# Optimization experiments

Measured on AMD Instinct MI355X. Metric: run time of the kernel, lower is better.

Reference implementation:

```python
import jax, jax.numpy as jnp
import numpy as np

EMB = 1024
HEADS = 16
DH = EMB // HEADS


def setup_inputs() -> dict:
    key = jax.random.key(0)
    ks = jax.random.split(key, 9)
    B, S = 4, 2048
    scale = 1.0 / np.sqrt(EMB)
    x = jax.random.normal(ks[0], (B, S, EMB), dtype=jnp.float32)
    Wq = jax.random.normal(ks[1], (EMB, EMB), dtype=jnp.float32) * scale
    Wk = jax.random.normal(ks[2], (EMB, EMB), dtype=jnp.float32) * scale
    Wv = jax.random.normal(ks[3], (EMB, EMB), dtype=jnp.float32) * scale
    Wo = jax.random.normal(ks[4], (EMB, EMB), dtype=jnp.float32) * scale
    bq = jnp.zeros((EMB,), jnp.float32)
    bk = jnp.zeros((EMB,), jnp.float32)
    bv = jnp.zeros((EMB,), jnp.float32)
    bo = jnp.zeros((EMB,), jnp.float32)
    return {"x": x, "Wq": Wq, "bq": bq, "Wk": Wk, "bk": bk,
            "Wv": Wv, "bv": bv, "Wo": Wo, "bo": bo}


def _split_heads(t):
    B, S, _ = t.shape
    return t.reshape(B, S, HEADS, DH).transpose(0, 2, 1, 3)  # [B,H,S,Dh]


def reference(x, Wq, bq, Wk, bk, Wv, bv, Wo, bo):
    q = _split_heads(x @ Wq + bq)
    k = _split_heads(x @ Wk + bk)
    v = _split_heads(x @ Wv + bv)
    # scaled dot-product attention, full [B,H,S,S] score matrix as in source
    logits = jnp.einsum("bhqd,bhkd->bhqk", q, k) / jnp.sqrt(jnp.float32(DH))
    attn = jax.nn.softmax(logits, axis=-1)
    ctx = jnp.einsum("bhqk,bhkd->bhqd", attn, v)
    B, _, S, _ = ctx.shape
    concat = ctx.transpose(0, 2, 1, 3).reshape(B, S, EMB)
    return concat @ Wo + bo
```

## Files before the change

kernel.cpp:

```cpp
#include <hip/hip_runtime.h>
#include <hip/hip_bf16.h>
#include <stdint.h>

typedef __bf16 bf16;
typedef __bf16 bf16x4 __attribute__((ext_vector_type(4)));
typedef __bf16 bf16x8 __attribute__((ext_vector_type(8)));
typedef float f32x4 __attribute__((ext_vector_type(4)));

__device__ __forceinline__ void async_ld16(const void* g, void* l) {
  __builtin_amdgcn_global_load_lds(
      (__attribute__((address_space(1))) void*)(void*)(g),
      (__attribute__((address_space(3))) void*)(l), 16, 0, 0);
}

__device__ __forceinline__ bf16 fast_bf16(float f) {
  uint32_t u = (__float_as_uint(f) + 0x8000u) >> 16;
  union { uint16_t s; bf16 b; } cv;
  cv.s = (uint16_t)u;
  return cv.b;
}

__device__ __forceinline__ uint32_t pack_bf16(float lo, float hi) {
  return __builtin_amdgcn_perm(__float_as_uint(hi) + 0x8000u,
                               __float_as_uint(lo) + 0x8000u, 0x07060302u);
}

__global__ __launch_bounds__(256) void cast_f32_bf16(const float* __restrict__ in,
                                                     bf16* __restrict__ out, int n) {
  int i = (blockIdx.x * 256 + threadIdx.x) * 4;
  if (i < n) {
    float4 f = *(const float4*)(in + i);
    uint2 o;
    o.x = pack_bf16(f.x, f.y);
    o.y = pack_bf16(f.z, f.w);
    *(uint2*)(out + i) = o;
  }
}

__global__ __launch_bounds__(256) void transpose_weights(const float* __restrict__ Wq,
                                                         const float* __restrict__ Wk,
                                                         const float* __restrict__ Wv,
                                                         const float* __restrict__ Wo,
                                                         bf16* __restrict__ Wt,
                                                         bf16* __restrict__ Wot) {
  __shared__ bf16 tile[64][66];
  int z = blockIdx.z;
  const float* src = z == 0 ? Wq : (z == 1 ? Wk : (z == 2 ? Wv : Wo));
  bf16* dst = z == 0 ? Wt : (z == 1 ? Wt + 1048576 : (z == 2 ? Wt + 2097152 : Wot));
  int r0 = blockIdx.x * 64, c0 = blockIdx.y * 64;
  int t = threadIdx.x;
#pragma unroll
  for (int i = 0; i < 16; ++i) {
    int idx = t + i * 256;
    int r = idx >> 6, c = idx & 63;
    tile[r][c] = fast_bf16(src[(size_t)(r0 + r) * 1024 + (c0 + c)]);
  }
  __syncthreads();
#pragma unroll
  for (int i = 0; i < 16; ++i) {
    int idx = t + i * 256;
    int c = idx >> 6, r = idx & 63;
    dst[(size_t)(c0 + c) * 1024 + (r0 + r)] = tile[r][c];
  }
}

__device__ __forceinline__ void gemm128_mainloop(const bf16* __restrict__ A,
                                                 const bf16* __restrict__ Bt, int K,
                                                 int rowBase, int colBase,
                                                 bf16* As, bf16* Bs,
                                                 f32x4 (&acc)[4][4]) {
  int t = threadIdx.x, lane = t & 63, w = t >> 6;
  int wM = w >> 1, wN = w & 1, quad = lane >> 4, l15 = lane & 15;
  int r_off = lane >> 3;
  int c_sw = (((lane & 7) ^ r_off) << 3);
  int sw = l15 & 7;
  for (int k0 = 0; k0 < K; k0 += 64) {
    __syncthreads();
#pragma unroll
    for (int i = 0; i < 4; ++i) {
      int e = i * 2048 + w * 512;
      int row = (e >> 6) + r_off;
      async_ld16(A + (size_t)(rowBase + row) * K + (k0 + c_sw), As + e);
      async_ld16(Bt + (size_t)(colBase + row) * K + (k0 + c_sw), Bs + e);
    }
    __syncthreads();
#pragma unroll
    for (int ks = 0; ks < 2; ++ks) {
      int co = (((ks * 4 + quad) ^ sw) << 3);
      bf16x8 af[4], bfr[4];
#pragma unroll
      for (int mi = 0; mi < 4; ++mi)
        af[mi] = *(const bf16x8*)(As + (wM * 64 + mi * 16 + l15) * 64 + co);
#pragma unroll
      for (int ni = 0; ni < 4; ++ni)
        bfr[ni] = *(const bf16x8*)(Bs + (wN * 64 + ni * 16 + l15) * 64 + co);
#pragma unroll
      for (int mi = 0; mi < 4; ++mi)
#pragma unroll
        for (int ni = 0; ni < 4; ++ni)
          acc[mi][ni] = __builtin_amdgcn_mfma_f32_16x16x32_bf16(af[mi], bfr[ni], acc[mi][ni], 0, 0, 0);
    }
  }
}

__global__ __launch_bounds__(256) void gemm_qkv(const bf16* __restrict__ X,
                                                const bf16* __restrict__ Wt,
                                                const float* __restrict__ bq,
                                                const float* __restrict__ bk,
                                                const float* __restrict__ bv,
                                                bf16* __restrict__ Qo,
                                                bf16* __restrict__ Ko,
                                                bf16* __restrict__ Vto) {
  __shared__ alignas(16) bf16 smem[2 * 128 * 64];
  bf16* As = smem;
  bf16* Bs = smem + 128 * 64;
  f32x4 acc[4][4];
  f32x4 z = {0.f, 0.f, 0.f, 0.f};
#pragma unroll
  for (int mi = 0; mi < 4; ++mi)
#pragma unroll
    for (int ni = 0; ni < 4; ++ni) acc[mi][ni] = z;
  int rowBase = blockIdx.y * 128, colBase = blockIdx.x * 128;
  gemm128_mainloop(X, Wt, 1024, rowBase, colBase, As, Bs, acc);

  int t = threadIdx.x, lane = t & 63, w = t >> 6;
  int wM = w >> 1, wN = w & 1, quad = lane >> 4, l15 = lane & 15;
  int which = colBase >> 10;
  int baseh = (colBase & 1023) >> 6;
  int b = rowBase >> 11, s0 = rowBase & 2047;

  if (which == 2) {
#pragma unroll
    for (int hp = 0; hp < 2; ++hp) {
      __syncthreads();
      if (wN == hp) {
#pragma unroll
        for (int mi = 0; mi < 4; ++mi)
#pragma unroll
          for (int ni = 0; ni < 4; ++ni) {
            int d = ni * 16 + l15;
            float bb = bv[(colBase & 1023) + hp * 64 + d];
            int sl = wM * 64 + mi * 16 + quad * 4;
            uint2 pv;
            pv.x = pack_bf16(acc[mi][ni][0] + bb, acc[mi][ni][1] + bb);
            pv.y = pack_bf16(acc[mi][ni][2] + bb, acc[mi][ni][3] + bb);
            *(uint2*)(smem + d * 136 + sl) = pv;
          }
      }
      __syncthreads();
      int hg = baseh + hp;
#pragma unroll
      for (int it = 0; it < 4; ++it) {
        int idx = t + it * 256;
        int d = idx >> 4, c = idx & 15;
        bf16x8 vv = *(const bf16x8*)(smem + d * 136 + c * 8);
        *(bf16x8*)(Vto + (((size_t)((b << 4) + hg) << 6) + d) * 2048 + s0 + c * 8) = vv;
      }
    }
  } else {
    const float* bias = which == 0 ? bq : bk;
    bf16* dst = which == 0 ? Qo : Ko;
    float scale = which == 0 ? 0.125f * 1.44269504f : 1.0f;
#pragma unroll
    for (int hp = 0; hp < 2; ++hp) {
      __syncthreads();
      if (wN == hp) {
#pragma unroll
        for (int mi = 0; mi < 4; ++mi)
#pragma unroll
          for (int ni = 0; ni < 4; ++ni) {
            int d = ni * 16 + l15;
            float bb = bias[(colBase & 1023) + hp * 64 + d];
            int m = wM * 64 + mi * 16 + quad * 4;
#pragma unroll
            for (int r = 0; r < 4; ++r)
              smem[(m + r) * 72 + d] = fast_bf16((acc[mi][ni][r] + bb) * scale);
          }
      }
      __syncthreads();
      int hg = baseh + hp;
      bf16* gbase = dst + ((((size_t)((b << 4) + hg)) * 2048 + s0) << 6);
#pragma unroll
      for (int it = 0; it < 4; ++it) {
        int idx = t + it * 256;
        int m = idx >> 3, c = idx & 7;
        bf16x8 vv = *(const bf16x8*)(smem + m * 72 + c * 8);
        *(bf16x8*)(gbase + m * 64 + c * 8) = vv;
      }
    }
  }
}

__global__ __launch_bounds__(256) void gemm_out(const bf16* __restrict__ Cb,
                                                const bf16* __restrict__ Wot,
                                                const float* __restrict__ bo,
                                                float* __restrict__ out) {
  __shared__ alignas(16) bf16 As[128 * 64];
  __shared__ alignas(16) bf16 Bs[128 * 64];
  f32x4 acc[4][4];
  f32x4 z = {0.f, 0.f, 0.f, 0.f};
#pragma unroll
  for (int mi = 0; mi < 4; ++mi)
#pragma unroll
    for (int ni = 0; ni < 4; ++ni) acc[mi][ni] = z;
  int rowBase = blockIdx.y * 128, colBase = blockIdx.x * 128;
  gemm128_mainloop(Cb, Wot, 1024, rowBase, colBase, As, Bs, acc);

  int t = threadIdx.x, lane = t & 63, w = t >> 6;
  int wM = w >> 1, wN = w & 1, quad = lane >> 4, l15 = lane & 15;
#pragma unroll
  for (int mi = 0; mi < 4; ++mi)
#pragma unroll
    for (int ni = 0; ni < 4; ++ni) {
      int n = colBase + wN * 64 + ni * 16 + l15;
      float bb = bo[n];
#pragma unroll
      for (int r = 0; r < 4; ++r) {
        int m = rowBase + wM * 64 + mi * 16 + quad * 4 + r;
        out[(size_t)m * 1024 + n] = acc[mi][ni][r] + bb;
      }
    }
}

__global__ __launch_bounds__(256, 2) void attn(const bf16* __restrict__ Q,
                                               const bf16* __restrict__ Kg,
                                               const bf16* __restrict__ Vt,
                                               bf16* __restrict__ ctx) {
  __shared__ alignas(16) bf16 QPs[256 * 64];
  __shared__ alignas(16) bf16 Ks[2][4096];
  __shared__ alignas(16) bf16 Vs[2][4096];

  int t = threadIdx.x, lane = t & 63, w = t >> 6;
  int quad = lane >> 4, l15 = lane & 15;
  int r_off = lane >> 3;
  int c_sw = (((lane & 7) ^ r_off) << 3);
  int sw = l15 & 7;
  int bh = blockIdx.x;
  int q0 = blockIdx.y * 256;
  const bf16* Qp = Q + ((size_t)bh * 2048 + q0) * 64;
  const bf16* Kp = Kg + (size_t)bh * 2048 * 64;
  const bf16* Vp = Vt + (size_t)bh * 64 * 2048;

#pragma unroll
  for (int i = 0; i < 8; ++i) {
    int e = w * 4096 + i * 512;
    int row = (e >> 6) + r_off;
    async_ld16(Qp + (size_t)row * 64 + c_sw, QPs + e);
  }
#pragma unroll
  for (int i = 0; i < 2; ++i) {
    int e = w * 1024 + i * 512;
    int row = (e >> 6) + r_off;
    async_ld16(Kp + (size_t)row * 64 + c_sw, Ks[0] + e);
    async_ld16(Vp + (size_t)row * 2048 + c_sw, Vs[0] + e);
  }
  __syncthreads();

  bf16x8 qf[2][4];
#pragma unroll
  for (int ks = 0; ks < 2; ++ks)
#pragma unroll
    for (int qi = 0; qi < 4; ++qi)
      qf[ks][qi] = *(const bf16x8*)(QPs + (w * 64 + qi * 16 + l15) * 64 + (((ks * 4 + quad) ^ sw) << 3));
  asm volatile("s_waitcnt lgkmcnt(0)" ::: "memory");

  bf16* Ps = QPs + w * 4096;

  bf16 one1 = (bf16)1.0f;
  bf16x8 ones = {one1, one1, one1, one1, one1, one1, one1, one1};

  f32x4 o[4][4];
  f32x4 ol[4];
  f32x4 z = {0.f, 0.f, 0.f, 0.f};
#pragma unroll
  for (int mi = 0; mi < 4; ++mi) {
    ol[mi] = z;
#pragma unroll
    for (int ni = 0; ni < 4; ++ni) o[mi][ni] = z;
  }

  for (int kt = 0; kt < 32; ++kt) {
    int cur = kt & 1;
    if (kt < 31) {
      int kn = (kt + 1) * 64;
#pragma unroll
      for (int i = 0; i < 2; ++i) {
        int e = w * 1024 + i * 512;
        int row = (e >> 6) + r_off;
        async_ld16(Kp + (size_t)(kn + row) * 64 + c_sw, Ks[cur ^ 1] + e);
        async_ld16(Vp + (size_t)row * 2048 + kn + c_sw, Vs[cur ^ 1] + e);
      }
    }
    const bf16* Kc = Ks[cur];
    const bf16* Vc = Vs[cur];

    f32x4 sA[2][4];
#pragma unroll
    for (int ki = 0; ki < 2; ++ki)
#pragma unroll
      for (int qi = 0; qi < 4; ++qi) sA[ki][qi] = z;
    __builtin_amdgcn_s_setprio(1);
#pragma unroll
    for (int ks = 0; ks < 2; ++ks) {
      int co = (((ks * 4 + quad) ^ sw) << 3);
      bf16x8 kf0 = *(const bf16x8*)(Kc + (l15) * 64 + co);
      bf16x8 kf1 = *(const bf16x8*)(Kc + (16 + l15) * 64 + co);
#pragma unroll
      for (int qi = 0; qi < 4; ++qi) {
        sA[0][qi] = __builtin_amdgcn_mfma_f32_16x16x32_bf16(kf0, qf[ks][qi], sA[0][qi], 0, 0, 0);
        sA[1][qi] = __builtin_amdgcn_mfma_f32_16x16x32_bf16(kf1, qf[ks][qi], sA[1][qi], 0, 0, 0);
      }
    }
    __builtin_amdgcn_s_setprio(0);
#pragma unroll
    for (int qi = 0; qi < 4; ++qi)
#pragma unroll
      for (int ki = 0; ki < 2; ++ki) {
        float p0 = __builtin_amdgcn_exp2f(sA[ki][qi][0]);
        float p1 = __builtin_amdgcn_exp2f(sA[ki][qi][1]);
        float p2 = __builtin_amdgcn_exp2f(sA[ki][qi][2]);
        float p3 = __builtin_amdgcn_exp2f(sA[ki][qi][3]);
        uint2 pb;
        pb.x = pack_bf16(p0, p1);
        pb.y = pack_bf16(p2, p3);
        int cs = (ki * 2 + (quad >> 1)) ^ sw;
        *(uint2*)(Ps + (qi * 16 + l15) * 64 + cs * 8 + (quad & 1) * 4) = pb;
      }

    f32x4 sB[2][4];
#pragma unroll
    for (int ki = 0; ki < 2; ++ki)
#pragma unroll
      for (int qi = 0; qi < 4; ++qi) sB[ki][qi] = z;
    __builtin_amdgcn_s_setprio(1);
#pragma unroll
    for (int ks = 0; ks < 2; ++ks) {
      int co = (((ks * 4 + quad) ^ sw) << 3);
      bf16x8 kf2 = *(const bf16x8*)(Kc + (32 + l15) * 64 + co);
      bf16x8 kf3 = *(const bf16x8*)(Kc + (48 + l15) * 64 + co);
#pragma unroll
      for (int qi = 0; qi < 4; ++qi) {
        sB[0][qi] = __builtin_amdgcn_mfma_f32_16x16x32_bf16(kf2, qf[ks][qi], sB[0][qi], 0, 0, 0);
        sB[1][qi] = __builtin_amdgcn_mfma_f32_16x16x32_bf16(kf3, qf[ks][qi], sB[1][qi], 0, 0, 0);
      }
    }
    __builtin_amdgcn_s_setprio(0);

    asm volatile("s_waitcnt lgkmcnt(0)" ::: "memory");

    {
      int co = ((quad ^ sw) << 3);
      bf16x8 pf[4], vf[4];
#pragma unroll
      for (int mi = 0; mi < 4; ++mi)
        pf[mi] = *(const bf16x8*)(Ps + (mi * 16 + l15) * 64 + co);
#pragma unroll
      for (int ni = 0; ni < 4; ++ni)
        vf[ni] = *(const bf16x8*)(Vc + (ni * 16 + l15) * 64 + co);
      __builtin_amdgcn_s_setprio(1);
#pragma unroll
      for (int mi = 0; mi < 4; ++mi) {
#pragma unroll
        for (int ni = 0; ni < 4; ++ni)
          o[mi][ni] = __builtin_amdgcn_mfma_f32_16x16x32_bf16(pf[mi], vf[ni], o[mi][ni], 0, 0, 0);
        ol[mi] = __builtin_amdgcn_mfma_f32_16x16x32_bf16(pf[mi], ones, ol[mi], 0, 0, 0);
      }
      __builtin_amdgcn_s_setprio(0);
    }

#pragma unroll
    for (int qi = 0; qi < 4; ++qi)
#pragma unroll
      for (int ki = 0; ki < 2; ++ki) {
        float p0 = __builtin_amdgcn_exp2f(sB[ki][qi][0]);
        float p1 = __builtin_amdgcn_exp2f(sB[ki][qi][1]);
        float p2 = __builtin_amdgcn_exp2f(sB[ki][qi][2]);
        float p3 = __builtin_amdgcn_exp2f(sB[ki][qi][3]);
        uint2 pb;
        pb.x = pack_bf16(p0, p1);
        pb.y = pack_bf16(p2, p3);
        int cs = (ki * 2 + 4 + (quad >> 1)) ^ sw;
        *(uint2*)(Ps + (qi * 16 + l15) * 64 + cs * 8 + (quad & 1) * 4) = pb;
      }

    asm volatile("s_waitcnt lgkmcnt(0)" ::: "memory");

    {
      int co = (((4 + quad) ^ sw) << 3);
      bf16x8 pf[4], vf[4];
#pragma unroll
      for (int mi = 0; mi < 4; ++mi)
        pf[mi] = *(const bf16x8*)(Ps + (mi * 16 + l15) * 64 + co);
#pragma unroll
      for (int ni = 0; ni < 4; ++ni)
        vf[ni] = *(const bf16x8*)(Vc + (ni * 16 + l15) * 64 + co);
      __builtin_amdgcn_s_setprio(1);
#pragma unroll
      for (int mi = 0; mi < 4; ++mi) {
#pragma unroll
        for (int ni = 0; ni < 4; ++ni)
          o[mi][ni] = __builtin_amdgcn_mfma_f32_16x16x32_bf16(pf[mi], vf[ni], o[mi][ni], 0, 0, 0);
        ol[mi] = __builtin_amdgcn_mfma_f32_16x16x32_bf16(pf[mi], ones, ol[mi], 0, 0, 0);
      }
      __builtin_amdgcn_s_setprio(0);
    }

    __syncthreads();
  }

  int b = bh >> 4, h = bh & 15;
#pragma unroll
  for (int mi = 0; mi < 4; ++mi) {
    float rl[4];
#pragma unroll
    for (int r = 0; r < 4; ++r) rl[r] = 1.0f / ol[mi][r];
#pragma unroll
    for (int ni = 0; ni < 4; ++ni) {
      int col = h * 64 + ni * 16 + l15;
#pragma unroll
      for (int r = 0; r < 4; ++r) {
        int q = q0 + w * 64 + mi * 16 + quad * 4 + r;
        ctx[(size_t)(b * 2048 + q) * 1024 + col] = fast_bf16(o[mi][ni][r] * rl[r]);
      }
    }
  }
}

extern "C" void kernel_launch(void* const* d_in, const int* in_sizes, int n_in,
                              void* d_out, int out_size, void* d_ws, size_t ws_size,
                              hipStream_t stream) {
  const float* x  = (const float*)d_in[0];
  const float* Wq = (const float*)d_in[1];
  const float* bq = (const float*)d_in[2];
  const float* Wk = (const float*)d_in[3];
  const float* bk = (const float*)d_in[4];
  const float* Wv = (const float*)d_in[5];
  const float* bv = (const float*)d_in[6];
  const float* Wo = (const float*)d_in[7];
  const float* bo = (const float*)d_in[8];
  float* out = (float*)d_out;

  char* ws = (char*)d_ws;
  const size_t MB = 1048576;
  bf16* xb  = (bf16*)(ws);
  bf16* Wt  = (bf16*)(ws + 16 * MB);
  bf16* Wot = (bf16*)(ws + 22 * MB);
  bf16* Qb  = (bf16*)(ws + 24 * MB);
  bf16* Kb  = (bf16*)(ws + 40 * MB);
  bf16* Vtb = (bf16*)(ws + 56 * MB);
  bf16* Cx  = (bf16*)(ws + 72 * MB);

  cast_f32_bf16<<<8192, 256, 0, stream>>>(x, xb, 8388608);
  transpose_weights<<<dim3(16, 16, 4), 256, 0, stream>>>(Wq, Wk, Wv, Wo, Wt, Wot);
  gemm_qkv<<<dim3(24, 64, 1), 256, 0, stream>>>(xb, Wt, bq, bk, bv, Qb, Kb, Vtb);
  attn<<<dim3(64, 8, 1), 256, 0, stream>>>(Qb, Kb, Vtb, Cx);
  gemm_out<<<dim3(8, 64, 1), 256, 0, stream>>>(Cx, Wot, bo, out);
}
```

Measured before the change: 280.6 us.

## Double-buffer QKV GEMM with 256x128 tiles and interleaved async loads

Reworks the QKV projection GEMM to use 256x128 output tiles with 512 threads. It double-buffers the A and B tiles in LDS and issues the next k-step's async global-to-LDS loads between MFMA sub-phases. MFMA bursts are wrapped in sched_barrier and setprio to keep the matrix units busy while loads are in flight. The epilogue is adapted to the larger tile. The aim is to hide global load latency and raise operand reuse per block, at the cost of about 96KB of LDS per block, which limits occupancy.

```diff
diff --git a/kernel.cpp b/kernel.cpp
--- a/kernel.cpp
+++ b/kernel.cpp
@@ -103,31 +103,143 @@
   }
 }
 
-__global__ __launch_bounds__(256) void gemm_qkv(const bf16* __restrict__ X,
-                                                const bf16* __restrict__ Wt,
-                                                const float* __restrict__ bq,
-                                                const float* __restrict__ bk,
-                                                const float* __restrict__ bv,
-                                                bf16* __restrict__ Qo,
-                                                bf16* __restrict__ Ko,
-                                                bf16* __restrict__ Vto) {
-  __shared__ alignas(16) bf16 smem[2 * 128 * 64];
-  bf16* As = smem;
-  bf16* Bs = smem + 128 * 64;
+__global__ __launch_bounds__(512, 2) void gemm_qkv(const bf16* __restrict__ X,
+                                                   const bf16* __restrict__ Wt,
+                                                   const float* __restrict__ bq,
+                                                   const float* __restrict__ bk,
+                                                   const float* __restrict__ bv,
+                                                   bf16* __restrict__ Qo,
+                                                   bf16* __restrict__ Ko,
+                                                   bf16* __restrict__ Vto) {
+  __shared__ alignas(16) bf16 smem[2][24576];
+
+  int t = threadIdx.x, lane = t & 63, w = t >> 6;
+  int wM = w >> 1, wN = w & 1, quad = lane >> 4, l15 = lane & 15;
+  int r_off = lane >> 3;
+  int c_sw = (((lane & 7) ^ r_off) << 3);
+  int sw = l15 & 7;
+  int rowBase = blockIdx.y * 256, colBase = blockIdx.x * 128;
+
   f32x4 acc[4][4];
   f32x4 z = {0.f, 0.f, 0.f, 0.f};
 #pragma unroll
   for (int mi = 0; mi < 4; ++mi)
 #pragma unroll
     for (int ni = 0; ni < 4; ++ni) acc[mi][ni] = z;
-  int rowBase = blockIdx.y * 128, colBase = blockIdx.x * 128;
-  gemm128_mainloop(X, Wt, 1024, rowBase, colBase, As, Bs, acc);
-
-  int t = threadIdx.x, lane = t & 63, w = t >> 6;
-  int wM = w >> 1, wN = w & 1, quad = lane >> 4, l15 = lane & 15;
+
+#pragma unroll
+  for (int i = 0; i < 4; ++i) {
+    int e = (w * 4 + i) * 512;
+    int row = (e >> 6) + r_off;
+    async_ld16(X + (size_t)(rowBase + row) * 1024 + c_sw, smem[0] + e);
+  }
+#pragma unroll
+  for (int i = 0; i < 2; ++i) {
+    int e = (w * 2 + i) * 512;
+    int row = (e >> 6) + r_off;
+    async_ld16(Wt + (size_t)(colBase + row) * 1024 + c_sw, smem[0] + 16384 + e);
+  }
+  __syncthreads();
+
+  for (int kt = 0; kt < 16; ++kt) {
+    int cur = kt & 1;
+    const bf16* As = smem[cur];
+    const bf16* Bs = smem[cur] + 16384;
+    bf16* Asn = smem[cur ^ 1];
+    bf16* Bsn = smem[cur ^ 1] + 16384;
+    int kn = (kt + 1) * 64;
+
+    bf16x8 af[4], bfr[2];
+
+    if (kt < 15) {
+#pragma unroll
+      for (int i = 0; i < 4; ++i) {
+        int e = (w * 4 + i) * 512;
+        int row = (e >> 6) + r_off;
+        async_ld16(X + (size_t)(rowBase + row) * 1024 + (kn + c_sw), Asn + e);
+      }
+    }
+    {
+      int co = ((quad ^ sw) << 3);
+#pragma unroll
+      for (int mi = 0; mi < 4; ++mi)
+        af[mi] = *(const bf16x8*)(As + (wM * 64 + mi * 16 + l15) * 64 + co);
+      bfr[0] = *(const bf16x8*)(Bs + (wN * 64 + l15) * 64 + co);
+      bfr[1] = *(const bf16x8*)(Bs + (wN * 64 + 16 + l15) * 64 + co);
+      asm volatile("s_waitcnt lgkmcnt(0)" ::: "memory");
+      __builtin_amdgcn_sched_barrier(0);
+      __builtin_amdgcn_s_setprio(1);
+#pragma unroll
+      for (int mi = 0; mi < 4; ++mi) {
+        acc[mi][0] = __builtin_amdgcn_mfma_f32_16x16x32_bf16(af[mi], bfr[0], acc[mi][0], 0, 0, 0);
+        acc[mi][1] = __builtin_amdgcn_mfma_f32_16x16x32_bf16(af[mi], bfr[1], acc[mi][1], 0, 0, 0);
+      }
+      __builtin_amdgcn_s_setprio(0);
+    }
+
+    if (kt < 15) {
+#pragma unroll
+      for (int i = 0; i < 2; ++i) {
+        int e = (w * 2 + i) * 512;
+        int row = (e >> 6) + r_off;
+        async_ld16(Wt + (size_t)(colBase + row) * 1024 + (kn + c_sw), Bsn + e);
+      }
+    }
+    {
+      int co = ((quad ^ sw) << 3);
+      bfr[0] = *(const bf16x8*)(Bs + (wN * 64 + 32 + l15) * 64 + co);
+      bfr[1] = *(const bf16x8*)(Bs + (wN * 64 + 48 + l15) * 64 + co);
+      asm volatile("s_waitcnt lgkmcnt(0)" ::: "memory");
+      __builtin_amdgcn_sched_barrier(0);
+      __builtin_amdgcn_s_setprio(1);
+#pragma unroll
+      for (int mi = 0; mi < 4; ++mi) {
+        acc[mi][2] = __builtin_amdgcn_mfma_f32_16x16x32_bf16(af[mi], bfr[0], acc[mi][2], 0, 0, 0);
+        acc[mi][3] = __builtin_amdgcn_mfma_f32_16x16x32_bf16(af[mi], bfr[1], acc[mi][3], 0, 0, 0);
+      }
+      __builtin_amdgcn_s_setprio(0);
+    }
+
+    {
+      int co = (((4 + quad) ^ sw) << 3);
+#pragma unroll
+      for (int mi = 0; mi < 4; ++mi)
+        af[mi] = *(const bf16x8*)(As + (wM * 64 + mi * 16 + l15) * 64 + co);
+      bfr[0] = *(const bf16x8*)(Bs + (wN * 64 + l15) * 64 + co);
+      bfr[1] = *(const bf16x8*)(Bs + (wN * 64 + 16 + l15) * 64 + co);
+      asm volatile("s_waitcnt lgkmcnt(0)" ::: "memory");
+      __builtin_amdgcn_sched_barrier(0);
+      __builtin_amdgcn_s_setprio(1);
+#pragma unroll
+      for (int mi = 0; mi < 4; ++mi) {
+        acc[mi][0] = __builtin_amdgcn_mfma_f32_16x16x32_bf16(af[mi], bfr[0], acc[mi][0], 0, 0, 0);
+        acc[mi][1] = __builtin_amdgcn_mfma_f32_16x16x32_bf16(af[mi], bfr[1], acc[mi][1], 0, 0, 0);
+      }
+      __builtin_amdgcn_s_setprio(0);
+    }
+
+    {
+      int co = (((4 + quad) ^ sw) << 3);
+      bfr[0] = *(const bf16x8*)(Bs + (wN * 64 + 32 + l15) * 64 + co);
+      bfr[1] = *(const bf16x8*)(Bs + (wN * 64 + 48 + l15) * 64 + co);
+      asm volatile("s_waitcnt lgkmcnt(0)" ::: "memory");
+      __builtin_amdgcn_sched_barrier(0);
+      __builtin_amdgcn_s_setprio(1);
+#pragma unroll
+      for (int mi = 0; mi < 4; ++mi) {
+        acc[mi][2] = __builtin_amdgcn_mfma_f32_16x16x32_bf16(af[mi], bfr[0], acc[mi][2], 0, 0, 0);
+        acc[mi][3] = __builtin_amdgcn_mfma_f32_16x16x32_bf16(af[mi], bfr[1], acc[mi][3], 0, 0, 0);
+      }
+      __builtin_amdgcn_s_setprio(0);
+    }
+
+    __syncthreads();
+  }
+
   int which = colBase >> 10;
   int baseh = (colBase & 1023) >> 6;
   int b = rowBase >> 11, s0 = rowBase & 2047;
+  bf16* ep = smem[0];
 
   if (which == 2) {
 #pragma unroll
@@ -144,16 +256,16 @@
             uint2 pv;
             pv.x = pack_bf16(acc[mi][ni][0] + bb, acc[mi][ni][1] + bb);
             pv.y = pack_bf16(acc[mi][ni][2] + bb, acc[mi][ni][3] + bb);
-            *(uint2*)(smem + d * 136 + sl) = pv;
+            *(uint2*)(ep + d * 264 + sl) = pv;
           }
       }
       __syncthreads();
       int hg = baseh + hp;
 #pragma unroll
       for (int it = 0; it < 4; ++it) {
-        int idx = t + it * 256;
-        int d = idx >> 4, c = idx & 15;
-        bf16x8 vv = *(const bf16x8*)(smem + d * 136 + c * 8);
+        int idx = t + it * 512;
+        int d = idx >> 5, c = idx & 31;
+        bf16x8 vv = *(const bf16x8*)(ep + d * 264 + c * 8);
         *(bf16x8*)(Vto + (((size_t)((b << 4) + hg) << 6) + d) * 2048 + s0 + c * 8) = vv;
       }
     }
@@ -174,7 +286,7 @@
             int m = wM * 64 + mi * 16 + quad * 4;
 #pragma unroll
             for (int r = 0; r < 4; ++r)
-              smem[(m + r) * 72 + d] = fast_bf16((acc[mi][ni][r] + bb) * scale);
+              ep[(m + r) * 72 + d] = fast_bf16((acc[mi][ni][r] + bb) * scale);
           }
       }
       __syncthreads();
@@ -182,9 +294,9 @@
       bf16* gbase = dst + ((((size_t)((b << 4) + hg)) * 2048 + s0) << 6);
 #pragma unroll
       for (int it = 0; it < 4; ++it) {
-        int idx = t + it * 256;
+        int idx = t + it * 512;
         int m = idx >> 3, c = idx & 7;
-        bf16x8 vv = *(const bf16x8*)(smem + m * 72 + c * 8);
+        bf16x8 vv = *(const bf16x8*)(ep + m * 72 + c * 8);
         *(bf16x8*)(gbase + m * 64 + c * 8) = vv;
       }
     }
@@ -452,7 +564,7 @@
 
   cast_f32_bf16<<<8192, 256, 0, stream>>>(x, xb, 8388608);
   transpose_weights<<<dim3(16, 16, 4), 256, 0, stream>>>(Wq, Wk, Wv, Wo, Wt, Wot);
-  gemm_qkv<<<dim3(24, 64, 1), 256, 0, stream>>>(xb, Wt, bq, bk, bv, Qb, Kb, Vtb);
+  gemm_qkv<<<dim3(24, 32, 1), 512, 0, stream>>>(xb, Wt, bq, bk, bv, Qb, Kb, Vtb);
   attn<<<dim3(64, 8, 1), 256, 0, stream>>>(Qb, Kb, Vtb, Cx);
   gemm_out<<<dim3(8, 64, 1), 256, 0, stream>>>(Cx, Wot, bo, out);
 }
```

Result: faster. 263.6 us (-6.1%).
